# Kernel optimization log

Hardware: AMD Instinct MI355X
Metric: run time of the kernel (lower is better)

Reference implementation:

```python
import jax, jax.numpy as jnp
import numpy as np

N = 10000          # nodes
E = 200000         # edges (avg degree 20)
LAT = 128          # latent dim
NEXP = 8           # experts
NTYPE = 95         # atom types (hard-coded 95x0e in module)
M0, M1, M2 = 128, 64, 32          # node/out irreps muls for l=0,1,2 (dim 480)
E0, E1, E2 = 64, 32, 16           # edge irreps muls (dim 240)
C0, C1, C2 = M0 + E0, M1 + E1, M2 + E2   # concat channels per l
T0 = M0 + M1 + M2                 # gate-input scalars: 128 scalars + 96 gates
AVG_NEIGH = 20.0


def setup_inputs() -> dict:
    key = jax.random.key(0)
    ks = jax.random.split(key, 32)
    r = lambda i, sh: jax.random.normal(ks[i], sh, dtype=jnp.float32)
    return {
        "latents": r(0, (E, LAT)),
        "node_features": r(1, (N, M0 + 3 * M1 + 5 * M2)),
        "edge_features": r(2, (E, E0 + 3 * E1 + 5 * E2)),
        "edge_vector": r(3, (E, 3)),
        "mole_globals": r(4, (LAT,)),
        "wigner_D1": r(5, (E, 3, 3)),
        "wigner_D2": r(6, (E, 5, 5)),
        "node_onehot": jax.nn.one_hot(jax.random.randint(ks[7], (N,), 0, NTYPE), NTYPE, dtype=jnp.float32),
        "Wg": r(8, (LAT, NEXP)),
        "Wm": r(9, (LAT, NEXP)),
        "W0_e": r(10, (NEXP, C0, T0)), "W0_s": r(11, (C0, T0)),
        "W1_e": r(12, (NEXP, C1, M1)), "W1_s": r(13, (C1, M1)),
        "W2_e": r(14, (NEXP, C2, M2)), "W2_s": r(15, (C2, M2)),
        "Wp0": r(16, (M0, M0)), "bp0": jnp.zeros((M0,), jnp.float32),
        "Wp1": r(17, (M1, M1)), "Wp2": r(18, (M2, M2)),
        "Wenv": r(19, (LAT, M0 + M1 + M2)),
        "Woh0": r(20, (M0, NTYPE)), "Woh1": r(21, (M1, NTYPE)), "Woh2": r(22, (M2, NTYPE)),
        "atom_type": jax.random.randint(ks[23], (N,), 0, NTYPE),
        "edge_index": jax.random.randint(ks[24], (2, E), 0, N),
        "active_edges": jnp.arange(E),
    }


def _mix(x, We, Ws, g):
    """Latent(expert)-conditioned per-l channel mixing: y = x @ (sum_e g_e W_e + W_shared).
    Loops over the small fixed expert count; never materializes per-edge weight matrices."""
    xm = x if x.ndim == 3 else x[:, :, None]           # [a, c, m]
    y = jnp.einsum('acm,co->aom', xm, Ws)
    for e in range(NEXP):
        y = y + g[:, e, None, None] * jnp.einsum('acm,co->aom', xm, We[e])
    y = y * float(1.0 / np.sqrt(xm.shape[1]))
    return y[:, :, 0] if x.ndim == 2 else y


def reference(latents, node_features, edge_features, edge_vector, mole_globals,
              wigner_D1, wigner_D2, node_onehot, Wg, Wm,
              W0_e, W0_s, W1_e, W1_s, W2_e, W2_s,
              Wp0, bp0, Wp1, Wp2, Wenv, Woh0, Woh1, Woh2,
              atom_type, edge_index, active_edges):
    edge_center = edge_index[0][active_edges]
    lat = latents[active_edges]
    # gather node features along edges, split irreps blocks
    xn = node_features[edge_center]                         # [Ea, 480]
    n0 = xn[:, :M0]
    n1 = xn[:, M0:M0 + 3 * M1].reshape(-1, M1, 3)
    n2 = xn[:, M0 + 3 * M1:].reshape(-1, M2, 5)
    e0 = edge_features[:, :E0]
    e1 = edge_features[:, E0:E0 + 3 * E1].reshape(-1, E1, 3)
    e2 = edge_features[:, E0 + 3 * E1:].reshape(-1, E2, 5)
    x0 = jnp.concatenate([n0, e0], axis=1)                  # [Ea, C0]
    x1 = jnp.concatenate([n1, e1], axis=1)                  # [Ea, C1, 3]
    x2 = jnp.concatenate([n2, e2], axis=1)                  # [Ea, C2, 5]
    # latent + molecular-global conditioned expert gates
    gates = jax.nn.softmax(lat @ Wg + mole_globals @ Wm, axis=-1)   # [Ea, NEXP]
    # SO(2)-style TP: rotate l>0 blocks into edge frame (Wigner-D), mix channels, rotate back
    x1r = jnp.einsum('amn,acn->acm', wigner_D1, x1)
    x2r = jnp.einsum('amn,acn->acm', wigner_D2, x2)
    t0 = _mix(x0, W0_e, W0_s, gates)                        # [Ea, T0]
    t1 = jnp.einsum('anm,aom->aon', wigner_D1, _mix(x1r, W1_e, W1_s, gates))
    t2 = jnp.einsum('anm,aom->aon', wigner_D2, _mix(x2r, W2_e, W2_s, gates))
    # Gate nonlinearity: silu scalars, sigmoid gates scale l>0 channels
    s = jax.nn.silu(t0[:, :M0])
    v1 = t1 * jax.nn.sigmoid(t0[:, M0:M0 + M1])[:, :, None]
    v2 = t2 * jax.nn.sigmoid(t0[:, M0 + M1:])[:, :, None]
    # lin_post: per-l equivariant linear (bias only on scalars), fan-in normalized
    s = s @ Wp0 * float(1.0 / np.sqrt(M0)) + bp0
    v1 = jnp.einsum('acm,co->aom', v1, Wp1) * float(1.0 / np.sqrt(M1))
    v2 = jnp.einsum('acm,co->aom', v2, Wp2) * float(1.0 / np.sqrt(M2))
    # E3ElementLinear: per-channel weights generated from latents
    w = lat @ Wenv * float(1.0 / np.sqrt(LAT))              # [Ea, M0+M1+M2]
    s = s * w[:, :M0]
    v1 = v1 * w[:, M0:M0 + M1, None]
    v2 = v2 * w[:, M0 + M1:, None]
    # scatter-reduce messages to nodes, normalize by rsqrt(avg_num_neighbors)
    norm = float(1.0 / np.sqrt(AVG_NEIGH))
    o0 = jax.ops.segment_sum(s, edge_center, num_segments=N) * norm
    o1 = jax.ops.segment_sum(v1, edge_center, num_segments=N) * norm
    o2 = jax.ops.segment_sum(v2, edge_center, num_segments=N) * norm
    # residual blend (res_update_params=0 -> u=sigmoid(0)=0.5), identity residual
    u = 0.5
    c_old = float(1.0 / np.sqrt(u * u + 1.0))
    c_new = u * c_old
    h0 = c_old * node_features[:, :M0] + c_new * o0
    h1 = c_old * node_features[:, M0:M0 + 3 * M1].reshape(N, M1, 3) + c_new * o1
    h2 = c_old * node_features[:, M0 + 3 * M1:].reshape(N, M2, 5) + c_new * o2
    # layer-onehot 'uvu' weighted TP with 95x0e, fan-in normalized, added residually
    invs = float(1.0 / np.sqrt(NTYPE))
    h0 = h0 + h0 * (node_onehot @ Woh0.T) * invs
    h1 = h1 + h1 * (node_onehot @ Woh1.T)[:, :, None] * invs
    h2 = h2 + h2 * (node_onehot @ Woh2.T)[:, :, None] * invs
    return jnp.concatenate([h0, h1.reshape(N, 3 * M1), h2.reshape(N, 5 * M2)], axis=1)
```

## Files before the change

### kernel.cpp

```cpp
#include <hip/hip_runtime.h>
#include <math.h>

namespace {

typedef __attribute__((ext_vector_type(8))) short short8;
typedef __attribute__((ext_vector_type(4))) float f32x4;

constexpr int kN   = 10000;
constexpr int kE   = 200000;
constexpr int kNT  = 95;
constexpr int kNFD = 480;

__device__ __forceinline__ ushort bf(float f) {
  union { float f; uint u; } c; c.f = f;
  uint r = c.u + 0x7FFF + ((c.u >> 16) & 1);
  return (ushort)(r >> 16);
}
__device__ __forceinline__ float fb(ushort u) {
  union { uint u; float f; } c; c.u = ((uint)u) << 16;
  return c.f;
}
__device__ __forceinline__ uint pk2(float a, float b) {
  return (uint)bf(a) | ((uint)bf(b) << 16);
}
// ... 282 lines not shown
          float av = (o < 128) ? (val/(1.f + __expf(-val)))
                               : (1.f/(1.f + __expf(-val)));
          outbf[(size_t)gr*N + o] = bf(av);
        } else {
          int a = gr/DIV;
          if (bias != nullptr) val += bias[o];
          float w = fb(wenvbf[(size_t)a*224 + WCOL + o]);
          val *= w*0.22360679774997896f;
          outbf[(size_t)gr*N + o] = bf(val);
        }
      }
    }
  }
}

template<int L>
__global__ __launch_bounds__(512)
void pv_k(const ushort* __restrict__ y, const ushort* __restrict__ t0act,
          const float* __restrict__ Dm, const ushort* __restrict__ Bpk,
          int rowsReal, float norm, const ushort* __restrict__ wenvbf,
          ushort* __restrict__ peout) {
  constexpr int DIV = (L == 1) ? 3 : 5;
  constexpr int K1  = (L == 1) ? 64 : 32;
  constexpr int NK  = K1/32;
  constexpr int N   = K1;
  constexpr int NT  = N/16;
  constexpr int CTW = NT/2;
  constexpr int LDA = K1 + 8;
  constexpr int WCOL = (L == 1) ? 128 : 192;
  constexpr int DSTR = (L == 1) ? 9 : 25;

  extern __shared__ char smraw[];
  ushort* Asm = (ushort*)smraw;

  const int tid = threadIdx.x;
  const int row0 = blockIdx.x*128;

  constexpr int C8 = K1/8;
  for (int u = tid; u < 128*C8; u += 512) {
    int r = u / C8, c8 = u - r*C8;
    int c0 = c8*8;
    int gr = row0 + r;
    uint4 v = {0u,0u,0u,0u};
    if (gr < rowsReal) {
      int a = gr/DIV, n = gr - a*DIV;
      const float* dd = Dm + (size_t)a*DSTR + n*DIV;
      short8 gt = *(const short8*)(t0act + (size_t)a*224 + WCOL + c0);
      float ov[8];
      if constexpr (L == 1) {
        short8 m0 = *(const short8*)(y + ((size_t)a*3 + 0)*64 + c0);
        short8 m1 = *(const short8*)(y + ((size_t)a*3 + 1)*64 + c0);
        short8 m2 = *(const short8*)(y + ((size_t)a*3 + 2)*64 + c0);
        float d0 = dd[0], d1 = dd[1], d2 = dd[2];
        #pragma unroll
        for (int j = 0; j < 8; ++j) {
          float s = d0*fb((ushort)m0[j]) + d1*fb((ushort)m1[j]) + d2*fb((ushort)m2[j]);
          ov[j] = s*fb((ushort)gt[j]);
        }
      } else {
        short8 m0 = *(const short8*)(y + ((size_t)a*5 + 0)*32 + c0);
        short8 m1 = *(const short8*)(y + ((size_t)a*5 + 1)*32 + c0);
        short8 m2 = *(const short8*)(y + ((size_t)a*5 + 2)*32 + c0);
        short8 m3 = *(const short8*)(y + ((size_t)a*5 + 3)*32 + c0);
        short8 m4 = *(const short8*)(y + ((size_t)a*5 + 4)*32 + c0);
        float d0 = dd[0], d1 = dd[1], d2 = dd[2], d3 = dd[3], d4 = dd[4];
        #pragma unroll
        for (int j = 0; j < 8; ++j) {
          float s = d0*fb((ushort)m0[j]) + d1*fb((ushort)m1[j])
                  + d2*fb((ushort)m2[j]) + d3*fb((ushort)m3[j])
                  + d4*fb((ushort)m4[j]);
          ov[j] = s*fb((ushort)gt[j]);
        }
      }
      v.x = pk2(ov[0], ov[1]); v.y = pk2(ov[2], ov[3]);
      v.z = pk2(ov[4], ov[5]); v.w = pk2(ov[6], ov[7]);
    }
    *(uint4*)(&Asm[r*LDA + c0]) = v;
  }
  __syncthreads();

  const int lane = tid & 63, wid = tid >> 6;
  const int cg = wid & 1, rg = wid >> 1;
  const int rbase = rg*32;
  const int lrow = lane & 15, lkb = lane >> 4;

  short8 af[2][NK];
  #pragma unroll
  for (int rt = 0; rt < 2; ++rt)
    #pragma unroll
    for (int kc = 0; kc < NK; ++kc)
      af[rt][kc] = *(const short8*)(&Asm[(rbase + rt*16 + lrow)*LDA + kc*32 + lkb*8]);

  f32x4 acc[2][CTW];
  #pragma unroll
  for (int rt = 0; rt < 2; ++rt)
    #pragma unroll
    for (int ct = 0; ct < CTW; ++ct)
      acc[rt][ct] = f32x4{0.f,0.f,0.f,0.f};

  __syncthreads();

  union BU { uint4 u; short8 s; };
  uint4* Bsm4 = (uint4*)smraw;
  const uint4* Bg4 = (const uint4*)Bpk;

  for (int u = tid; u < NT*NK*64; u += 512)
    Bsm4[u] = Bg4[u];
  __syncthreads();

  #pragma unroll
  for (int ct = 0; ct < CTW; ++ct) {
    int nt = cg*CTW + ct;
    #pragma unroll
    for (int kc = 0; kc < NK; ++kc) {
      BU b; b.u = Bsm4[(nt*NK + kc)*64 + lane];
      acc[0][ct] = __builtin_amdgcn_mfma_f32_16x16x32_bf16(af[0][kc], b.s, acc[0][ct], 0, 0, 0);
      acc[1][ct] = __builtin_amdgcn_mfma_f32_16x16x32_bf16(af[1][kc], b.s, acc[1][ct], 0, 0, 0);
    }
  }

  #pragma unroll
  for (int rt = 0; rt < 2; ++rt) {
    #pragma unroll
    for (int ct = 0; ct < CTW; ++ct) {
      #pragma unroll
      for (int q = 0; q < 4; ++q) {
        int gr = row0 + rbase + rt*16 + lkb*4 + q;
        if (gr >= rowsReal) continue;
        int o = (cg*CTW + ct)*16 + lrow;
        int a = gr/DIV;
        float val = acc[rt][ct][q]*norm;
        float w = fb(wenvbf[(size_t)a*224 + WCOL + o]);
        val *= w*0.22360679774997896f;
        peout[(size_t)gr*N + o] = bf(val);
      }
    }
  }
}

constexpr int T0SMB = 55808;

template<int C>
__device__ __forceinline__ void t0_phase(int e, int tid, int lane, int cg,
                                         int rbase, int lkb,
                                         const short8 (&af)[2][6],
                                         f32x4 (&acc)[2][7],
                                         const float* coefsm,
                                         uint4* Bsm4, const uint4* Bg4,
                                         uint4& rg0, uint4& rg1, uint4& rg2) {
  fastbar();
  const bool hasNext = !(e == 8 && C == 3);
  if (hasNext) {
    int ne = e + (C == 3 ? 1 : 0);
    int nc = (C + 1) & 3;
    const uint4* s = Bg4 + (size_t)ne*6144 + (size_t)nc*1536;
    rg0 = s[tid]; rg1 = s[tid + 512]; rg2 = s[tid + 1024];
  }
  float cf[2][4];
  #pragma unroll
  for (int rt = 0; rt < 2; ++rt)
    #pragma unroll
    for (int q = 0; q < 4; ++q)
      cf[rt][q] = coefsm[(rbase + rt*16 + lkb*4 + q)*9 + e];
  union BU { uint4 u; short8 s; };
  const uint4* bb = Bsm4 + (C & 1)*1536;
  {
    f32x4 z0 = {0.f,0.f,0.f,0.f}, z1 = {0.f,0.f,0.f,0.f};
    #pragma unroll
    for (int kc = 0; kc < 6; ++kc) {
      BU b; b.u = bb[(cg*6 + kc)*64 + lane];
      z0 = __builtin_amdgcn_mfma_f32_16x16x32_bf16(af[0][kc], b.s, z0, 0, 0, 0);
      z1 = __builtin_amdgcn_mfma_f32_16x16x32_bf16(af[1][kc], b.s, z1, 0, 0, 0);
    }
    #pragma unroll
    for (int q = 0; q < 4; ++q) {
      acc[0][2*C][q] += cf[0][q]*z0[q];
      acc[1][2*C][q] += cf[1][q]*z1[q];
    }
  }
  if constexpr (2*C + 1 < 7) {
    f32x4 z0 = {0.f,0.f,0.f,0.f}, z1 = {0.f,0.f,0.f,0.f};
    #pragma unroll
    for (int kc = 0; kc < 6; ++kc) {
      BU b; b.u = bb[((2 + cg)*6 + kc)*64 + lane];
      z0 = __builtin_amdgcn_mfma_f32_16x16x32_bf16(af[0][kc], b.s, z0, 0, 0, 0);
      z1 = __builtin_amdgcn_mfma_f32_16x16x32_bf16(af[1][kc], b.s, z1, 0, 0, 0);
    }
    #pragma unroll
    for (int q = 0; q < 4; ++q) {
      acc[0][2*C + 1][q] += cf[0][q]*z0[q];
      acc[1][2*C + 1][q] += cf[1][q]*z1[q];
    }
  }
  fastbar();
  if (hasNext) {
    uint4* d = Bsm4 + ((C + 1) & 1)*1536;
    d[tid] = rg0; d[tid + 512] = rg1; d[tid + 1024] = rg2;
  }
}

__global__ __launch_bounds__(512, 2)
void t0c_k(const float* __restrict__ nodef, const float* __restrict__ edgef,
           const int* __restrict__ eidx, const int* __restrict__ act,
           const ushort* __restrict__ Bpk, const ushort* __restrict__ Bp0,
           const float* __restrict__ coefg, const float* __restrict__ bp0f,
           const ushort* __restrict__ wenvbf,
           ushort* __restrict__ t0act, ushort* __restrict__ pe0) {
  extern __shared__ char smraw[];
  __shared__ int cenl[128];
  ushort* Asm = (ushort*)smraw;
  float* coefsm = (float*)(smraw + 51200);
  uint4* Bsm4 = (uint4*)smraw;
  const uint4* Bg4 = (const uint4*)Bpk;

  const int tid = threadIdx.x;
  const int row0 = blockIdx.x*128;

  if (tid < 128) {
    int gr = row0 + tid;
    cenl[tid] = (gr < kE) ? eidx[act[gr]] : 0;
  }
  __syncthreads();

  for (int u = tid; u < 128*24; u += 512) {
    int r = u/24, g = u - r*24;
    int c0 = g*8;
    int gr = row0 + r;
    uint4 v = {0u,0u,0u,0u};
    if (gr < kE) {
      const float* s = (g < 16) ? (nodef + (size_t)cenl[r]*kNFD + c0)
                                : (edgef + (size_t)gr*240 + (c0 - 128));
      float4 f0 = *(const float4*)s;
      float4 f1 = *(const float4*)(s + 4);
      v.x = pk2(f0.x, f0.y); v.y = pk2(f0.z, f0.w);
      v.z = pk2(f1.x, f1.y); v.w = pk2(f1.z, f1.w);
    }
    *(uint4*)(&Asm[r*200 + c0]) = v;
  }
  for (int u = tid; u < 128*9; u += 512) {
    int r = u/9, e = u - r*9;
    coefsm[r*9 + e] = coefg[(size_t)(row0 + r)*9 + e];
  }
  __syncthreads();

  const int lane = tid & 63, wid = tid >> 6;
  const int cg = wid & 1, rg = wid >> 1;
  const int rbase = rg*32;
  const int lrow = lane & 15, lkb = lane >> 4;

  short8 af[2][6];
  #pragma unroll
  for (int rt = 0; rt < 2; ++rt)
    #pragma unroll
    for (int kc = 0; kc < 6; ++kc)
      af[rt][kc] = *(const short8*)(&Asm[(rbase + rt*16 + lrow)*200 + kc*32 + lkb*8]);

  f32x4 acc[2][7];
  #pragma unroll
  for (int rt = 0; rt < 2; ++rt)
    #pragma unroll
    for (int ct = 0; ct < 7; ++ct)
      acc[rt][ct] = f32x4{0.f,0.f,0.f,0.f};

  __syncthreads();

  uint4 rg0, rg1, rg2;
  { const uint4* s = Bg4; rg0 = s[tid]; rg1 = s[tid + 512]; rg2 = s[tid + 1024]; }
  { uint4* d = Bsm4;      d[tid] = rg0; d[tid + 512] = rg1; d[tid + 1024] = rg2; }

  for (int e = 0; e < 9; ++e) {
    t0_phase<0>(e, tid, lane, cg, rbase, lkb, af, acc, coefsm, Bsm4, Bg4, rg0, rg1, rg2);
    t0_phase<1>(e, tid, lane, cg, rbase, lkb, af, acc, coefsm, Bsm4, Bg4, rg0, rg1, rg2);
    t0_phase<2>(e, tid, lane, cg, rbase, lkb, af, acc, coefsm, Bsm4, Bg4, rg0, rg1, rg2);
    t0_phase<3>(e, tid, lane, cg, rbase, lkb, af, acc, coefsm, Bsm4, Bg4, rg0, rg1, rg2);
  }

  ushort* A2 = (ushort*)smraw;
  #pragma unroll
  for (int rt = 0; rt < 2; ++rt) {
    #pragma unroll
    for (int ct = 0; ct < 7; ++ct) {
      int o = (2*ct + cg)*16 + lrow;
      #pragma unroll
      for (int q = 0; q < 4; ++q) {
        int rloc = rbase + rt*16 + lkb*4 + q;
        int gr = row0 + rloc;
        float val = acc[rt][ct][q]*0.07216878364870323f;
        if (o < 128) {
          A2[rloc*136 + o] = bf(val/(1.f + __expf(-val)));
        } else if (gr < kE) {
          t0act[(size_t)gr*224 + o] = bf(1.f/(1.f + __expf(-val)));
        }
      }
    }
  }
  fastbar();

  short8 af2[2][4];
  #pragma unroll
  for (int rt = 0; rt < 2; ++rt)
    #pragma unroll
    for (int kc = 0; kc < 4; ++kc)
      af2[rt][kc] = *(const short8*)(&A2[(rbase + rt*16 + lrow)*136 + kc*32 + lkb*8]);

  union BU { uint4 u; short8 s; };
  const uint4* Bg0 = (const uint4*)Bp0;
  f32x4 acc2[2][4];
  #pragma unroll
  for (int rt = 0; rt < 2; ++rt)
    #pragma unroll
    for (int ct = 0; ct < 4; ++ct)
      acc2[rt][ct] = f32x4{0.f,0.f,0.f,0.f};

  #pragma unroll
  for (int ct = 0; ct < 4; ++ct) {
    int nt = cg*4 + ct;
    #pragma unroll
    for (int kc = 0; kc < 4; ++kc) {
      BU b; b.u = Bg0[(nt*4 + kc)*64 + lane];
      acc2[0][ct] = __builtin_amdgcn_mfma_f32_16x16x32_bf16(af2[0][kc], b.s, acc2[0][ct], 0, 0, 0);
      acc2[1][ct] = __builtin_amdgcn_mfma_f32_16x16x32_bf16(af2[1][kc], b.s, acc2[1][ct], 0, 0, 0);
    }
  }

  #pragma unroll
  for (int rt = 0; rt < 2; ++rt) {
    #pragma unroll
    for (int ct = 0; ct < 4; ++ct) {
      int o = (cg*4 + ct)*16 + lrow;
      float bia = bp0f[o];
      #pragma unroll
      for (int q = 0; q < 4; ++q) {
        int gr = row0 + rbase + rt*16 + lkb*4 + q;
        if (gr >= kE) continue;
        float v = acc2[rt][ct][q]*0.08838834764831845f + bia;
        v *= fb(wenvbf[(size_t)gr*224 + o])*0.22360679774997896f;
        pe0[(size_t)gr*128 + o] = bf(v);
      }
    }
  }
}

constexpr int ych_smbytes(int K1, int NK, int NT) {
  int a = 128*(K1 + 8)*2;
  int b = 2*NT*NK*1024;
  int u = a > b ? a : b;
  return u + 128*9*4;
}

template<int DIV, int K1, int NK, int NT, int FUSE>
__global__ __launch_bounds__(512, 2)
void ychunk_k(const float* __restrict__ nodef, const float* __restrict__ edgef,
              const float* __restrict__ Dm, const int* __restrict__ eidx,
              const int* __restrict__ act, const ushort* __restrict__ Bpk,
              const float* __restrict__ coefg, int rowsReal, float norm,
              ushort* __restrict__ outbf) {
  constexpr int CTW = NT/2;
  constexpr int N   = NT*16;
  constexpr int LDA = K1 + 8;
  constexpr int ABYTES = 128*LDA*2;
  constexpr int BBYTES = 2*NT*NK*1024;
  constexpr int UNI = (ABYTES > BBYTES) ? ABYTES : BBYTES;
  constexpr int NB4 = NT*NK*64;
  constexpr int DSTR = (FUSE == 1) ? 9 : 25;

  extern __shared__ char smraw[];
  ushort* Asm = (ushort*)smraw;
  float* coefsm = (float*)(smraw + UNI);
  uint4* Bsm4 = (uint4*)smraw;
  const uint4* Bg4 = (const uint4*)Bpk;

  const int tid = threadIdx.x;
  const int row0 = blockIdx.x*128;

  constexpr int C8 = K1/8;
  for (int u = tid; u < 128*C8; u += 512) {
    int r = u / C8, c8 = u - r*C8;
    int c0 = c8*8;
    int gr = row0 + r;
    uint4 v = {0u,0u,0u,0u};
    if (gr < rowsReal) {
      int a = gr/DIV, mm = gr - a*DIV;
      int cen = eidx[act[a]];
      const float* dd = Dm + (size_t)a*DSTR + mm*DIV;
      if constexpr (FUSE == 1) {
        const float* s = (c8 < 8) ? (nodef + (size_t)cen*kNFD + 128 + c0*3)
                                  : (edgef + (size_t)a*240 + 64 + (c0 - 64)*3);
        float ld[24];
        #pragma unroll
        for (int q = 0; q < 6; ++q)
          *(float4*)(ld + q*4) = *(const float4*)(s + q*4);
        float d0 = dd[0], d1 = dd[1], d2 = dd[2];
        float ov[8];
        #pragma unroll
        for (int j = 0; j < 8; ++j)
          ov[j] = d0*ld[3*j] + d1*ld[3*j + 1] + d2*ld[3*j + 2];
        v.x = pk2(ov[0], ov[1]); v.y = pk2(ov[2], ov[3]);
        v.z = pk2(ov[4], ov[5]); v.w = pk2(ov[6], ov[7]);
      } else {
        if (c0 < 48) {
// ... 77 lines not shown
      }
      #pragma unroll
      for (int q = 0; q < 4; ++q) {
        acc[0][ct][q] += cf[0][q]*z0[q];
        acc[1][ct][q] += cf[1][q]*z1[q];
      }
    }
    fastbar();
    if (e + 1 < 9) {
      uint4* d = Bsm4 + ((e + 1) & 1)*NB4;
      if (tid < NB4) d[tid] = pf0;
      if constexpr (NB4 > 512) { if (tid + 512 < NB4) d[tid + 512] = pf1; }
    }
  }

  #pragma unroll
  for (int rt = 0; rt < 2; ++rt) {
    #pragma unroll
    for (int ct = 0; ct < CTW; ++ct) {
      #pragma unroll
      for (int q = 0; q < 4; ++q) {
        int gr = row0 + rbase + rt*16 + lkb*4 + q;
        if (gr >= rowsReal) continue;
        int o = (cg*CTW + ct)*16 + lrow;
        outbf[(size_t)gr*N + o] = bf(acc[rt][ct][q]*norm);
      }
    }
  }
}

__global__ __launch_bounds__(256)
void gather_k(const float* __restrict__ nodef, const float* __restrict__ onehot,
              const float* __restrict__ Woh0, const float* __restrict__ Woh1,
              const float* __restrict__ Woh2,
              const int* __restrict__ rowptr, const int* __restrict__ elist,
              const ushort* __restrict__ pe0, const ushort* __restrict__ pe1,
              const ushort* __restrict__ pe2, float* __restrict__ out) {
  __shared__ int tn;
  const int n = blockIdx.x;
  const int t = threadIdx.x;
// ... 27 lines not shown
    if (j < 128)      f = Woh0[j*kNT + ty];
    else if (j < 320) f = Woh1[((j - 128)/3)*kNT + ty];
    else              f = Woh2[((j - 320)/5)*kNT + ty];
    out[idx] = h*(1.f + f*invs);
  }
}

constexpr size_t OFF_CNT  = 0;
constexpr size_t OFF_CUR  = 40000;
constexpr size_t OFF_RP   = 80000;
constexpr size_t OFF_EL   = 120064;
constexpr size_t OFF_PACK = 1000000;
constexpr size_t OFF_COEF = 19200000;
constexpr size_t OFF_MGL  = 26402304;
constexpr size_t OFF_PE0  = 168031232;
constexpr size_t OFF_X2R  = 219264000;
constexpr size_t OFF_WENV = 347272192;
constexpr size_t OFF_T0A  = 436900864;
constexpr size_t OFF_Y1   = 526529536;
constexpr size_t OFF_Y2   = 603354112;

}

extern "C" void kernel_launch(void* const* d_in, const int* in_sizes, int n_in,
                              void* d_out, int out_size, void* d_ws, size_t ws_size,
                              hipStream_t stream) {
  (void)in_sizes; (void)n_in; (void)out_size; (void)ws_size;
  const float* latents = (const float*)d_in[0];
  const float* nodef   = (const float*)d_in[1];
  const float* edgef   = (const float*)d_in[2];
  const float* mg      = (const float*)d_in[4];
  const float* D1      = (const float*)d_in[5];
  const float* D2      = (const float*)d_in[6];
  const float* onehot  = (const float*)d_in[7];
  const float* Wg      = (const float*)d_in[8];
// ... 13 lines not shown
  const float* Woh1    = (const float*)d_in[22];
  const float* Woh2    = (const float*)d_in[23];
  const int* eidx      = (const int*)d_in[25];
  const int* act       = (const int*)d_in[26];

  char* ws = (char*)d_ws;
  int*    cnt   = (int*)(ws + OFF_CNT);
  int*    cur   = (int*)(ws + OFF_CUR);
  int*    rp    = (int*)(ws + OFF_RP);
  int*    el    = (int*)(ws + OFF_EL);
  ushort* pk    = (ushort*)(ws + OFF_PACK);
  float*  coef  = (float*)(ws + OFF_COEF);
  float*  mgl   = (float*)(ws + OFF_MGL);
  ushort* wenv  = (ushort*)(ws + OFF_WENV);
  ushort* t0act = (ushort*)(ws + OFF_T0A);
  ushort* y1    = (ushort*)(ws + OFF_Y1);
  ushort* y2    = (ushort*)(ws + OFF_Y2);
  ushort* pe0   = (ushort*)(ws + OFF_PE0);
  ushort* pe1   = (ushort*)(ws + OFF_X2R);
  ushort* pe2   = (ushort*)(ws + OFF_Y1);
  float*  out   = (float*)d_out;

  hipMemsetAsync(cnt, 0, kN*sizeof(int), stream);
  hist_k<<<(kE + 255)/256, 256, 0, stream>>>(eidx, act, cnt);
  scan_k<<<1, 256, 0, stream>>>(cnt, rp, cur);
  scatter_k<<<(kE + 255)/256, 256, 0, stream>>>(eidx, act, cur, el);

  pack_k<<<(PKTOT + 255)/256, 256, 0, stream>>>(W0e, W0s, W1e, W1s, W2e, W2s,
                                                Wenv, Wp0, Wp1, Wp2, pk);
  mgl_k<<<1, 64, 0, stream>>>(mg, Wm, mgl);

  coef_k<<<kE/32, 256, 0, stream>>>(latents, mgl, Wg, act, coef);

  {
    auto kp = gemm_k<1,128,4,224,1,0,true>;
    int smb = gemm_smbytes(128,4,224,1);
    hipFuncSetAttribute((const void*)kp, hipFuncAttributeMaxDynamicSharedMemorySize, smb);
    kp<<<1563, 512, smb, stream>>>(
        nullptr, latents, act, 128, pk + PKENV, nullptr, kE, 0.08838834764831845f,
        wenv, nullptr, nullptr, 0);
  }
  {
    auto kp = ychunk_k<3,96,3,4,1>;
    int smb = ych_smbytes(96,3,4);
    hipFuncSetAttribute((const void*)kp, hipFuncAttributeMaxDynamicSharedMemorySize, smb);
    kp<<<4688, 512, smb, stream>>>(
        nodef, edgef, D1, eidx, act, pk + PK1, coef, 3*kE,
        0.10206207261596577f, y1);
  }
  {
    auto kp = ychunk_k<5,64,2,2,2>;
    int smb = ych_smbytes(64,2,2);
    hipFuncSetAttribute((const void*)kp, hipFuncAttributeMaxDynamicSharedMemorySize, smb);
    kp<<<7813, 512, smb, stream>>>(
        nodef, edgef, D2, eidx, act, pk + PK2, coef, 5*kE,
        0.14433756729740643f, y2);
  }

  {
    hipFuncSetAttribute((const void*)t0c_k,
                        hipFuncAttributeMaxDynamicSharedMemorySize, T0SMB);
    t0c_k<<<1563, 512, T0SMB, stream>>>(nodef, edgef, eidx, act,
                                        pk + PK0, pk + PKP0, coef,
                                        bp0, wenv, t0act, pe0);
  }

  {
    auto kp = pv_k<1>;
    int smb = gemm_smbytes(64,2,64,1);
    hipFuncSetAttribute((const void*)kp, hipFuncAttributeMaxDynamicSharedMemorySize, smb);
    kp<<<4688, 512, smb, stream>>>(
        y1, t0act, D1, pk + PKP1, 3*kE, 0.125f, wenv, pe1);
  }
  {
    auto kp = pv_k<2>;
    int smb = gemm_smbytes(32,1,32,1);
    hipFuncSetAttribute((const void*)kp, hipFuncAttributeMaxDynamicSharedMemorySize, smb);
    kp<<<7813, 512, smb, stream>>>(
        y2, t0act, D2, pk + PKP2, 5*kE, 0.17677669529663687f, wenv, pe2);
  }

  gather_k<<<kN, 256, 0, stream>>>(nodef, onehot, Woh0, Woh1, Woh2,
                                   rp, el, pe0, pe1, pe2, out);
}
```

Baseline: 1.272 ms.

## Fuse expert-mix chunk GEMM with rotate-back projection for l=1,2 paths

Merges the ychunk kernels (expert-weighted mixing of l=1/l=2 channels) with the pv kernels (Wigner back-rotation, gating, post-projection and envelope scaling) into one ypv kernel per l. The intermediate y tensors now stay in shared memory instead of round-tripping through global memory. To keep each edge's m-components inside one block, blocks cover 126 or 125 rows (multiples of 3 or 5) rather than 128, so a few MFMA rows are wasted. Occupancy is capped at one block per CU via launch bounds, and the larger shared footprint may reduce latency hiding.

```diff
diff --git a/kernel.cpp b/kernel.cpp
--- a/kernel.cpp
+++ b/kernel.cpp
@@ -320,27 +320,54 @@
   }
 }
 
+constexpr int ypv_smbytes(int K1, int NK, int NT) {
+  int a = 128*(K1 + 8)*2;
+  int b = 2*NT*NK*1024;
+  int y = 128*(NT*16 + 8)*2;
+  int u = a > b ? a : b;
+  u = u > y ? u : y;
+  return u + 128*9*4;
+}
+
 template<int L>
-__global__ __launch_bounds__(512)
-void pv_k(const ushort* __restrict__ y, const ushort* __restrict__ t0act,
-          const float* __restrict__ Dm, const ushort* __restrict__ Bpk,
-          int rowsReal, float norm, const ushort* __restrict__ wenvbf,
-          ushort* __restrict__ peout) {
-  constexpr int DIV = (L == 1) ? 3 : 5;
-  constexpr int K1  = (L == 1) ? 64 : 32;
-  constexpr int NK  = K1/32;
-  constexpr int N   = K1;
-  constexpr int NT  = N/16;
-  constexpr int CTW = NT/2;
-  constexpr int LDA = K1 + 8;
+__global__ __launch_bounds__(512, 1)
+void ypv_k(const float* __restrict__ nodef, const float* __restrict__ edgef,
+           const float* __restrict__ Dm, const int* __restrict__ eidx,
+           const int* __restrict__ act, const ushort* __restrict__ Bpk,
+           const ushort* __restrict__ Bp, const float* __restrict__ coefg,
+           const ushort* __restrict__ t0act, const ushort* __restrict__ wenvbf,
+           ushort* __restrict__ peout) {
+  constexpr int DIV  = (L == 1) ? 3 : 5;
+  constexpr int K1   = (L == 1) ? 96 : 64;
+  constexpr int NK   = K1/32;
+  constexpr int NT   = (L == 1) ? 4 : 2;
+  constexpr int N    = NT*16;
+  constexpr int CTW  = NT/2;
+  constexpr int LDA  = K1 + 8;
+  constexpr int RR   = (L == 1) ? 126 : 125;
+  constexpr int DSTR = (L == 1) ? 9 : 25;
   constexpr int WCOL = (L == 1) ? 128 : 192;
-  constexpr int DSTR = (L == 1) ? 9 : 25;
+  constexpr int NB4  = NT*NK*64;
+  constexpr int LDY  = N + 8;
+  constexpr int NK2  = N/32;
+  constexpr int ABYTES = 128*LDA*2;
+  constexpr int BBYTES = 2*NB4*16;
+  constexpr int UNI0 = (ABYTES > BBYTES) ? ABYTES : BBYTES;
+  constexpr int YBYTES = 128*LDY*2;
+  constexpr int UNI = (UNI0 > YBYTES) ? UNI0 : YBYTES;
+
+  const float norm1 = (L == 1) ? 0.10206207261596577f : 0.14433756729740643f;
+  const float norm2 = (L == 1) ? 0.125f : 0.17677669529663687f;
+  const int rowsTotal = (L == 1) ? 3*kE : 5*kE;
 
   extern __shared__ char smraw[];
   ushort* Asm = (ushort*)smraw;
+  float* coefsm = (float*)(smraw + UNI);
+  uint4* Bsm4 = (uint4*)smraw;
+  const uint4* Bg4 = (const uint4*)Bpk;
 
   const int tid = threadIdx.x;
-  const int row0 = blockIdx.x*128;
+  const int row0 = blockIdx.x*RR;
 
   constexpr int C8 = K1/8;
   for (int u = tid; u < 128*C8; u += 512) {
@@ -348,348 +375,11 @@
     int c0 = c8*8;
     int gr = row0 + r;
     uint4 v = {0u,0u,0u,0u};
-    if (gr < rowsReal) {
-      int a = gr/DIV, n = gr - a*DIV;
-      const float* dd = Dm + (size_t)a*DSTR + n*DIV;
-      short8 gt = *(const short8*)(t0act + (size_t)a*224 + WCOL + c0);
-      float ov[8];
-      if constexpr (L == 1) {
-        short8 m0 = *(const short8*)(y + ((size_t)a*3 + 0)*64 + c0);
-        short8 m1 = *(const short8*)(y + ((size_t)a*3 + 1)*64 + c0);
-        short8 m2 = *(const short8*)(y + ((size_t)a*3 + 2)*64 + c0);
-        float d0 = dd[0], d1 = dd[1], d2 = dd[2];
-        #pragma unroll
-        for (int j = 0; j < 8; ++j) {
-          float s = d0*fb((ushort)m0[j]) + d1*fb((ushort)m1[j]) + d2*fb((ushort)m2[j]);
-          ov[j] = s*fb((ushort)gt[j]);
-        }
-      } else {
-        short8 m0 = *(const short8*)(y + ((size_t)a*5 + 0)*32 + c0);
-        short8 m1 = *(const short8*)(y + ((size_t)a*5 + 1)*32 + c0);
-        short8 m2 = *(const short8*)(y + ((size_t)a*5 + 2)*32 + c0);
-        short8 m3 = *(const short8*)(y + ((size_t)a*5 + 3)*32 + c0);
-        short8 m4 = *(const short8*)(y + ((size_t)a*5 + 4)*32 + c0);
-        float d0 = dd[0], d1 = dd[1], d2 = dd[2], d3 = dd[3], d4 = dd[4];
-        #pragma unroll
-        for (int j = 0; j < 8; ++j) {
-          float s = d0*fb((ushort)m0[j]) + d1*fb((ushort)m1[j])
-                  + d2*fb((ushort)m2[j]) + d3*fb((ushort)m3[j])
-                  + d4*fb((ushort)m4[j]);
-          ov[j] = s*fb((ushort)gt[j]);
-        }
-      }
-      v.x = pk2(ov[0], ov[1]); v.y = pk2(ov[2], ov[3]);
-      v.z = pk2(ov[4], ov[5]); v.w = pk2(ov[6], ov[7]);
-    }
-    *(uint4*)(&Asm[r*LDA + c0]) = v;
-  }
-  __syncthreads();
-
-  const int lane = tid & 63, wid = tid >> 6;
-  const int cg = wid & 1, rg = wid >> 1;
-  const int rbase = rg*32;
-  const int lrow = lane & 15, lkb = lane >> 4;
-
-  short8 af[2][NK];
-  #pragma unroll
-  for (int rt = 0; rt < 2; ++rt)
-    #pragma unroll
-    for (int kc = 0; kc < NK; ++kc)
-      af[rt][kc] = *(const short8*)(&Asm[(rbase + rt*16 + lrow)*LDA + kc*32 + lkb*8]);
-
-  f32x4 acc[2][CTW];
-  #pragma unroll
-  for (int rt = 0; rt < 2; ++rt)
-    #pragma unroll
-    for (int ct = 0; ct < CTW; ++ct)
-      acc[rt][ct] = f32x4{0.f,0.f,0.f,0.f};
-
-  __syncthreads();
-
-  union BU { uint4 u; short8 s; };
-  uint4* Bsm4 = (uint4*)smraw;
-  const uint4* Bg4 = (const uint4*)Bpk;
-
-  for (int u = tid; u < NT*NK*64; u += 512)
-    Bsm4[u] = Bg4[u];
-  __syncthreads();
-
-  #pragma unroll
-  for (int ct = 0; ct < CTW; ++ct) {
-    int nt = cg*CTW + ct;
-    #pragma unroll
-    for (int kc = 0; kc < NK; ++kc) {
-      BU b; b.u = Bsm4[(nt*NK + kc)*64 + lane];
-      acc[0][ct] = __builtin_amdgcn_mfma_f32_16x16x32_bf16(af[0][kc], b.s, acc[0][ct], 0, 0, 0);
-      acc[1][ct] = __builtin_amdgcn_mfma_f32_16x16x32_bf16(af[1][kc], b.s, acc[1][ct], 0, 0, 0);
-    }
-  }
-
-  #pragma unroll
-  for (int rt = 0; rt < 2; ++rt) {
-    #pragma unroll
-    for (int ct = 0; ct < CTW; ++ct) {
-      #pragma unroll
-      for (int q = 0; q < 4; ++q) {
-        int gr = row0 + rbase + rt*16 + lkb*4 + q;
-        if (gr >= rowsReal) continue;
-        int o = (cg*CTW + ct)*16 + lrow;
-        int a = gr/DIV;
-        float val = acc[rt][ct][q]*norm;
-        float w = fb(wenvbf[(size_t)a*224 + WCOL + o]);
-        val *= w*0.22360679774997896f;
-        peout[(size_t)gr*N + o] = bf(val);
-      }
-    }
-  }
-}
-
-constexpr int T0SMB = 55808;
-
-template<int C>
-__device__ __forceinline__ void t0_phase(int e, int tid, int lane, int cg,
-                                         int rbase, int lkb,
-                                         const short8 (&af)[2][6],
-                                         f32x4 (&acc)[2][7],
-                                         const float* coefsm,
-                                         uint4* Bsm4, const uint4* Bg4,
-                                         uint4& rg0, uint4& rg1, uint4& rg2) {
-  fastbar();
-  const bool hasNext = !(e == 8 && C == 3);
-  if (hasNext) {
-    int ne = e + (C == 3 ? 1 : 0);
-    int nc = (C + 1) & 3;
-    const uint4* s = Bg4 + (size_t)ne*6144 + (size_t)nc*1536;
-    rg0 = s[tid]; rg1 = s[tid + 512]; rg2 = s[tid + 1024];
-  }
-  float cf[2][4];
-  #pragma unroll
-  for (int rt = 0; rt < 2; ++rt)
-    #pragma unroll
-    for (int q = 0; q < 4; ++q)
-      cf[rt][q] = coefsm[(rbase + rt*16 + lkb*4 + q)*9 + e];
-  union BU { uint4 u; short8 s; };
-  const uint4* bb = Bsm4 + (C & 1)*1536;
-  {
-    f32x4 z0 = {0.f,0.f,0.f,0.f}, z1 = {0.f,0.f,0.f,0.f};
-    #pragma unroll
-    for (int kc = 0; kc < 6; ++kc) {
-      BU b; b.u = bb[(cg*6 + kc)*64 + lane];
-      z0 = __builtin_amdgcn_mfma_f32_16x16x32_bf16(af[0][kc], b.s, z0, 0, 0, 0);
-      z1 = __builtin_amdgcn_mfma_f32_16x16x32_bf16(af[1][kc], b.s, z1, 0, 0, 0);
-    }
-    #pragma unroll
-    for (int q = 0; q < 4; ++q) {
-      acc[0][2*C][q] += cf[0][q]*z0[q];
-      acc[1][2*C][q] += cf[1][q]*z1[q];
-    }
-  }
-  if constexpr (2*C + 1 < 7) {
-    f32x4 z0 = {0.f,0.f,0.f,0.f}, z1 = {0.f,0.f,0.f,0.f};
-    #pragma unroll
-    for (int kc = 0; kc < 6; ++kc) {
-      BU b; b.u = bb[((2 + cg)*6 + kc)*64 + lane];
-      z0 = __builtin_amdgcn_mfma_f32_16x16x32_bf16(af[0][kc], b.s, z0, 0, 0, 0);
-      z1 = __builtin_amdgcn_mfma_f32_16x16x32_bf16(af[1][kc], b.s, z1, 0, 0, 0);
-    }
-    #pragma unroll
-    for (int q = 0; q < 4; ++q) {
-      acc[0][2*C + 1][q] += cf[0][q]*z0[q];
-      acc[1][2*C + 1][q] += cf[1][q]*z1[q];
-    }
-  }
-  fastbar();
-  if (hasNext) {
-    uint4* d = Bsm4 + ((C + 1) & 1)*1536;
-    d[tid] = rg0; d[tid + 512] = rg1; d[tid + 1024] = rg2;
-  }
-}
-
-__global__ __launch_bounds__(512, 2)
-void t0c_k(const float* __restrict__ nodef, const float* __restrict__ edgef,
-           const int* __restrict__ eidx, const int* __restrict__ act,
-           const ushort* __restrict__ Bpk, const ushort* __restrict__ Bp0,
-           const float* __restrict__ coefg, const float* __restrict__ bp0f,
-           const ushort* __restrict__ wenvbf,
-           ushort* __restrict__ t0act, ushort* __restrict__ pe0) {
-  extern __shared__ char smraw[];
-  __shared__ int cenl[128];
-  ushort* Asm = (ushort*)smraw;
-  float* coefsm = (float*)(smraw + 51200);
-  uint4* Bsm4 = (uint4*)smraw;
-  const uint4* Bg4 = (const uint4*)Bpk;
-
-  const int tid = threadIdx.x;
-  const int row0 = blockIdx.x*128;
-
-  if (tid < 128) {
-    int gr = row0 + tid;
-    cenl[tid] = (gr < kE) ? eidx[act[gr]] : 0;
-  }
-  __syncthreads();
-
-  for (int u = tid; u < 128*24; u += 512) {
-    int r = u/24, g = u - r*24;
-    int c0 = g*8;
-    int gr = row0 + r;
-    uint4 v = {0u,0u,0u,0u};
-    if (gr < kE) {
-      const float* s = (g < 16) ? (nodef + (size_t)cenl[r]*kNFD + c0)
-                                : (edgef + (size_t)gr*240 + (c0 - 128));
-      float4 f0 = *(const float4*)s;
-      float4 f1 = *(const float4*)(s + 4);
-      v.x = pk2(f0.x, f0.y); v.y = pk2(f0.z, f0.w);
-      v.z = pk2(f1.x, f1.y); v.w = pk2(f1.z, f1.w);
-    }
-    *(uint4*)(&Asm[r*200 + c0]) = v;
-  }
-  for (int u = tid; u < 128*9; u += 512) {
-    int r = u/9, e = u - r*9;
-    coefsm[r*9 + e] = coefg[(size_t)(row0 + r)*9 + e];
-  }
-  __syncthreads();
-
-  const int lane = tid & 63, wid = tid >> 6;
-  const int cg = wid & 1, rg = wid >> 1;
-  const int rbase = rg*32;
-  const int lrow = lane & 15, lkb = lane >> 4;
-
-  short8 af[2][6];
-  #pragma unroll
-  for (int rt = 0; rt < 2; ++rt)
-    #pragma unroll
-    for (int kc = 0; kc < 6; ++kc)
-      af[rt][kc] = *(const short8*)(&Asm[(rbase + rt*16 + lrow)*200 + kc*32 + lkb*8]);
-
-  f32x4 acc[2][7];
-  #pragma unroll
-  for (int rt = 0; rt < 2; ++rt)
-    #pragma unroll
-    for (int ct = 0; ct < 7; ++ct)
-      acc[rt][ct] = f32x4{0.f,0.f,0.f,0.f};
-
-  __syncthreads();
-
-  uint4 rg0, rg1, rg2;
-  { const uint4* s = Bg4; rg0 = s[tid]; rg1 = s[tid + 512]; rg2 = s[tid + 1024]; }
-  { uint4* d = Bsm4;      d[tid] = rg0; d[tid + 512] = rg1; d[tid + 1024] = rg2; }
-
-  for (int e = 0; e < 9; ++e) {
-    t0_phase<0>(e, tid, lane, cg, rbase, lkb, af, acc, coefsm, Bsm4, Bg4, rg0, rg1, rg2);
-    t0_phase<1>(e, tid, lane, cg, rbase, lkb, af, acc, coefsm, Bsm4, Bg4, rg0, rg1, rg2);
-    t0_phase<2>(e, tid, lane, cg, rbase, lkb, af, acc, coefsm, Bsm4, Bg4, rg0, rg1, rg2);
-    t0_phase<3>(e, tid, lane, cg, rbase, lkb, af, acc, coefsm, Bsm4, Bg4, rg0, rg1, rg2);
-  }
-
-  ushort* A2 = (ushort*)smraw;
-  #pragma unroll
-  for (int rt = 0; rt < 2; ++rt) {
-    #pragma unroll
-    for (int ct = 0; ct < 7; ++ct) {
-      int o = (2*ct + cg)*16 + lrow;
-      #pragma unroll
-      for (int q = 0; q < 4; ++q) {
-        int rloc = rbase + rt*16 + lkb*4 + q;
-        int gr = row0 + rloc;
-        float val = acc[rt][ct][q]*0.07216878364870323f;
-        if (o < 128) {
-          A2[rloc*136 + o] = bf(val/(1.f + __expf(-val)));
-        } else if (gr < kE) {
-          t0act[(size_t)gr*224 + o] = bf(1.f/(1.f + __expf(-val)));
-        }
-      }
-    }
-  }
-  fastbar();
-
-  short8 af2[2][4];
-  #pragma unroll
-  for (int rt = 0; rt < 2; ++rt)
-    #pragma unroll
-    for (int kc = 0; kc < 4; ++kc)
-      af2[rt][kc] = *(const short8*)(&A2[(rbase + rt*16 + lrow)*136 + kc*32 + lkb*8]);
-
-  union BU { uint4 u; short8 s; };
-  const uint4* Bg0 = (const uint4*)Bp0;
-  f32x4 acc2[2][4];
-  #pragma unroll
-  for (int rt = 0; rt < 2; ++rt)
-    #pragma unroll
-    for (int ct = 0; ct < 4; ++ct)
-      acc2[rt][ct] = f32x4{0.f,0.f,0.f,0.f};
-
-  #pragma unroll
-  for (int ct = 0; ct < 4; ++ct) {
-    int nt = cg*4 + ct;
-    #pragma unroll
-    for (int kc = 0; kc < 4; ++kc) {
-      BU b; b.u = Bg0[(nt*4 + kc)*64 + lane];
-      acc2[0][ct] = __builtin_amdgcn_mfma_f32_16x16x32_bf16(af2[0][kc], b.s, acc2[0][ct], 0, 0, 0);
-      acc2[1][ct] = __builtin_amdgcn_mfma_f32_16x16x32_bf16(af2[1][kc], b.s, acc2[1][ct], 0, 0, 0);
-    }
-  }
-
-  #pragma unroll
-  for (int rt = 0; rt < 2; ++rt) {
-    #pragma unroll
-    for (int ct = 0; ct < 4; ++ct) {
-      int o = (cg*4 + ct)*16 + lrow;
-      float bia = bp0f[o];
-      #pragma unroll
-      for (int q = 0; q < 4; ++q) {
-        int gr = row0 + rbase + rt*16 + lkb*4 + q;
-        if (gr >= kE) continue;
-        float v = acc2[rt][ct][q]*0.08838834764831845f + bia;
-        v *= fb(wenvbf[(size_t)gr*224 + o])*0.22360679774997896f;
-        pe0[(size_t)gr*128 + o] = bf(v);
-      }
-    }
-  }
-}
-
-constexpr int ych_smbytes(int K1, int NK, int NT) {
-  int a = 128*(K1 + 8)*2;
-  int b = 2*NT*NK*1024;
-  int u = a > b ? a : b;
-  return u + 128*9*4;
-}
-
-template<int DIV, int K1, int NK, int NT, int FUSE>
-__global__ __launch_bounds__(512, 2)
-void ychunk_k(const float* __restrict__ nodef, const float* __restrict__ edgef,
-              const float* __restrict__ Dm, const int* __restrict__ eidx,
-              const int* __restrict__ act, const ushort* __restrict__ Bpk,
-              const float* __restrict__ coefg, int rowsReal, float norm,
-              ushort* __restrict__ outbf) {
-  constexpr int CTW = NT/2;
-  constexpr int N   = NT*16;
-  constexpr int LDA = K1 + 8;
-  constexpr int ABYTES = 128*LDA*2;
-  constexpr int BBYTES = 2*NT*NK*1024;
-  constexpr int UNI = (ABYTES > BBYTES) ? ABYTES : BBYTES;
-  constexpr int NB4 = NT*NK*64;
-  constexpr int DSTR = (FUSE == 1) ? 9 : 25;
-
-  extern __shared__ char smraw[];
-  ushort* Asm = (ushort*)smraw;
-  float* coefsm = (float*)(smraw + UNI);
-  uint4* Bsm4 = (uint4*)smraw;
-  const uint4* Bg4 = (const uint4*)Bpk;
-
-  const int tid = threadIdx.x;
-  const int row0 = blockIdx.x*128;
-
-  constexpr int C8 = K1/8;
-  for (int u = tid; u < 128*C8; u += 512) {
-    int r = u / C8, c8 = u - r*C8;
-    int c0 = c8*8;
-    int gr = row0 + r;
-    uint4 v = {0u,0u,0u,0u};
-    if (gr < rowsReal) {
+    if (gr < rowsTotal) {
       int a = gr/DIV, mm = gr - a*DIV;
       int cen = eidx[act[a]];
       const float* dd = Dm + (size_t)a*DSTR + mm*DIV;
-      if constexpr (FUSE == 1) {
+      if constexpr (L == 1) {
         const float* s = (c8 < 8) ? (nodef + (size_t)cen*kNFD + 128 + c0*3)
                                   : (edgef + (size_t)a*240 + 64 + (c0 - 64)*3);
         float ld[24];
@@ -797,16 +487,300 @@
     }
   }
 
+  ushort* yl = (ushort*)smraw;
   #pragma unroll
   for (int rt = 0; rt < 2; ++rt) {
     #pragma unroll
     for (int ct = 0; ct < CTW; ++ct) {
+      int o = (cg*CTW + ct)*16 + lrow;
+      #pragma unroll
+      for (int q = 0; q < 4; ++q) {
+        int r = rbase + rt*16 + lkb*4 + q;
+        yl[r*LDY + o] = bf(acc[rt][ct][q]*norm1);
+      }
+    }
+  }
+  fastbar();
+
+  short8 af2[2][NK2];
+  #pragma unroll
+  for (int rt = 0; rt < 2; ++rt) {
+    int r2 = rbase + rt*16 + lrow;
+    int gr = row0 + r2;
+    bool valid = (r2 < RR) && (gr < rowsTotal);
+    float dd[DIV];
+    int rb = 0;
+    const ushort* gtp = nullptr;
+    if (valid) {
+      int a = gr/DIV, n = gr - a*DIV;
+      rb = r2 - n;
+      #pragma unroll
+      for (int m = 0; m < DIV; ++m) dd[m] = Dm[(size_t)a*DSTR + n*DIV + m];
+      gtp = t0act + (size_t)a*224 + WCOL;
+    }
+    #pragma unroll
+    for (int kc = 0; kc < NK2; ++kc) {
+      int c0 = kc*32 + lkb*8;
+      short8 frag = {0,0,0,0,0,0,0,0};
+      if (valid) {
+        short8 gt = *(const short8*)(gtp + c0);
+        float ov[8];
+        #pragma unroll
+        for (int j = 0; j < 8; ++j) ov[j] = 0.f;
+        #pragma unroll
+        for (int m = 0; m < DIV; ++m) {
+          short8 ym = *(const short8*)(&yl[(rb + m)*LDY + c0]);
+          #pragma unroll
+          for (int j = 0; j < 8; ++j) ov[j] += dd[m]*fb((ushort)ym[j]);
+        }
+        uint4 pkd;
+        pkd.x = pk2(ov[0]*fb((ushort)gt[0]), ov[1]*fb((ushort)gt[1]));
+        pkd.y = pk2(ov[2]*fb((ushort)gt[2]), ov[3]*fb((ushort)gt[3]));
+        pkd.z = pk2(ov[4]*fb((ushort)gt[4]), ov[5]*fb((ushort)gt[5]));
+        pkd.w = pk2(ov[6]*fb((ushort)gt[6]), ov[7]*fb((ushort)gt[7]));
+        union { uint4 u; short8 s; } cv; cv.u = pkd;
+        frag = cv.s;
+      }
+      af2[rt][kc] = frag;
+    }
+  }
+
+  const uint4* Bgp = (const uint4*)Bp;
+  f32x4 acc2[2][CTW];
+  #pragma unroll
+  for (int rt = 0; rt < 2; ++rt)
+    #pragma unroll
+    for (int ct = 0; ct < CTW; ++ct)
+      acc2[rt][ct] = f32x4{0.f,0.f,0.f,0.f};
+
+  #pragma unroll
+  for (int ct = 0; ct < CTW; ++ct) {
+    int nt = cg*CTW + ct;
+    #pragma unroll
+    for (int kc = 0; kc < NK2; ++kc) {
+      BU b; b.u = Bgp[(nt*NK2 + kc)*64 + lane];
+      acc2[0][ct] = __builtin_amdgcn_mfma_f32_16x16x32_bf16(af2[0][kc], b.s, acc2[0][ct], 0, 0, 0);
+      acc2[1][ct] = __builtin_amdgcn_mfma_f32_16x16x32_bf16(af2[1][kc], b.s, acc2[1][ct], 0, 0, 0);
+    }
+  }
+
+  #pragma unroll
+  for (int rt = 0; rt < 2; ++rt) {
+    #pragma unroll
+    for (int ct = 0; ct < CTW; ++ct) {
+      int o = (cg*CTW + ct)*16 + lrow;
+      #pragma unroll
+      for (int q = 0; q < 4; ++q) {
+        int r2 = rbase + rt*16 + lkb*4 + q;
+        int gr = row0 + r2;
+        if (r2 >= RR || gr >= rowsTotal) continue;
+        int a = gr/DIV;
+        float val = acc2[rt][ct][q]*norm2;
+        val *= fb(wenvbf[(size_t)a*224 + WCOL + o])*0.22360679774997896f;
+        peout[(size_t)gr*N + o] = bf(val);
+      }
+    }
+  }
+}
+
+constexpr int T0SMB = 55808;
+
+template<int C>
+__device__ __forceinline__ void t0_phase(int e, int tid, int lane, int cg,
+                                         int rbase, int lkb,
+                                         const short8 (&af)[2][6],
+                                         f32x4 (&acc)[2][7],
+                                         const float* coefsm,
+                                         uint4* Bsm4, const uint4* Bg4,
+                                         uint4& rg0, uint4& rg1, uint4& rg2) {
+  fastbar();
+  const bool hasNext = !(e == 8 && C == 3);
+  if (hasNext) {
+    int ne = e + (C == 3 ? 1 : 0);
+    int nc = (C + 1) & 3;
+    const uint4* s = Bg4 + (size_t)ne*6144 + (size_t)nc*1536;
+    rg0 = s[tid]; rg1 = s[tid + 512]; rg2 = s[tid + 1024];
+  }
+  float cf[2][4];
+  #pragma unroll
+  for (int rt = 0; rt < 2; ++rt)
+    #pragma unroll
+    for (int q = 0; q < 4; ++q)
+      cf[rt][q] = coefsm[(rbase + rt*16 + lkb*4 + q)*9 + e];
+  union BU { uint4 u; short8 s; };
+  const uint4* bb = Bsm4 + (C & 1)*1536;
+  {
+    f32x4 z0 = {0.f,0.f,0.f,0.f}, z1 = {0.f,0.f,0.f,0.f};
+    #pragma unroll
+    for (int kc = 0; kc < 6; ++kc) {
+      BU b; b.u = bb[(cg*6 + kc)*64 + lane];
+      z0 = __builtin_amdgcn_mfma_f32_16x16x32_bf16(af[0][kc], b.s, z0, 0, 0, 0);
+      z1 = __builtin_amdgcn_mfma_f32_16x16x32_bf16(af[1][kc], b.s, z1, 0, 0, 0);
+    }
+    #pragma unroll
+    for (int q = 0; q < 4; ++q) {
+      acc[0][2*C][q] += cf[0][q]*z0[q];
+      acc[1][2*C][q] += cf[1][q]*z1[q];
+    }
+  }
+  if constexpr (2*C + 1 < 7) {
+    f32x4 z0 = {0.f,0.f,0.f,0.f}, z1 = {0.f,0.f,0.f,0.f};
+    #pragma unroll
+    for (int kc = 0; kc < 6; ++kc) {
+      BU b; b.u = bb[((2 + cg)*6 + kc)*64 + lane];
+      z0 = __builtin_amdgcn_mfma_f32_16x16x32_bf16(af[0][kc], b.s, z0, 0, 0, 0);
+      z1 = __builtin_amdgcn_mfma_f32_16x16x32_bf16(af[1][kc], b.s, z1, 0, 0, 0);
+    }
+    #pragma unroll
+    for (int q = 0; q < 4; ++q) {
+      acc[0][2*C + 1][q] += cf[0][q]*z0[q];
+      acc[1][2*C + 1][q] += cf[1][q]*z1[q];
+    }
+  }
+  fastbar();
+  if (hasNext) {
+    uint4* d = Bsm4 + ((C + 1) & 1)*1536;
+    d[tid] = rg0; d[tid + 512] = rg1; d[tid + 1024] = rg2;
+  }
+}
+
+__global__ __launch_bounds__(512, 2)
+void t0c_k(const float* __restrict__ nodef, const float* __restrict__ edgef,
+           const int* __restrict__ eidx, const int* __restrict__ act,
+           const ushort* __restrict__ Bpk, const ushort* __restrict__ Bp0,
+           const float* __restrict__ coefg, const float* __restrict__ bp0f,
+           const ushort* __restrict__ wenvbf,
+           ushort* __restrict__ t0act, ushort* __restrict__ pe0) {
+  extern __shared__ char smraw[];
+  __shared__ int cenl[128];
+  ushort* Asm = (ushort*)smraw;
+  float* coefsm = (float*)(smraw + 51200);
+  uint4* Bsm4 = (uint4*)smraw;
+  const uint4* Bg4 = (const uint4*)Bpk;
+
+  const int tid = threadIdx.x;
+  const int row0 = blockIdx.x*128;
+
+  if (tid < 128) {
+    int gr = row0 + tid;
+    cenl[tid] = (gr < kE) ? eidx[act[gr]] : 0;
+  }
+  __syncthreads();
+
+  for (int u = tid; u < 128*24; u += 512) {
+    int r = u/24, g = u - r*24;
+    int c0 = g*8;
+    int gr = row0 + r;
+    uint4 v = {0u,0u,0u,0u};
+    if (gr < kE) {
+      const float* s = (g < 16) ? (nodef + (size_t)cenl[r]*kNFD + c0)
+                                : (edgef + (size_t)gr*240 + (c0 - 128));
+      float4 f0 = *(const float4*)s;
+      float4 f1 = *(const float4*)(s + 4);
+      v.x = pk2(f0.x, f0.y); v.y = pk2(f0.z, f0.w);
+      v.z = pk2(f1.x, f1.y); v.w = pk2(f1.z, f1.w);
+    }
+    *(uint4*)(&Asm[r*200 + c0]) = v;
+  }
+  for (int u = tid; u < 128*9; u += 512) {
+    int r = u/9, e = u - r*9;
+    coefsm[r*9 + e] = coefg[(size_t)(row0 + r)*9 + e];
+  }
+  __syncthreads();
+
+  const int lane = tid & 63, wid = tid >> 6;
+  const int cg = wid & 1, rg = wid >> 1;
+  const int rbase = rg*32;
+  const int lrow = lane & 15, lkb = lane >> 4;
+
+  short8 af[2][6];
+  #pragma unroll
+  for (int rt = 0; rt < 2; ++rt)
+    #pragma unroll
+    for (int kc = 0; kc < 6; ++kc)
+      af[rt][kc] = *(const short8*)(&Asm[(rbase + rt*16 + lrow)*200 + kc*32 + lkb*8]);
+
+  f32x4 acc[2][7];
+  #pragma unroll
+  for (int rt = 0; rt < 2; ++rt)
+    #pragma unroll
+    for (int ct = 0; ct < 7; ++ct)
+      acc[rt][ct] = f32x4{0.f,0.f,0.f,0.f};
+
+  __syncthreads();
+
+  uint4 rg0, rg1, rg2;
+  { const uint4* s = Bg4; rg0 = s[tid]; rg1 = s[tid + 512]; rg2 = s[tid + 1024]; }
+  { uint4* d = Bsm4;      d[tid] = rg0; d[tid + 512] = rg1; d[tid + 1024] = rg2; }
+
+  for (int e = 0; e < 9; ++e) {
+    t0_phase<0>(e, tid, lane, cg, rbase, lkb, af, acc, coefsm, Bsm4, Bg4, rg0, rg1, rg2);
+    t0_phase<1>(e, tid, lane, cg, rbase, lkb, af, acc, coefsm, Bsm4, Bg4, rg0, rg1, rg2);
+    t0_phase<2>(e, tid, lane, cg, rbase, lkb, af, acc, coefsm, Bsm4, Bg4, rg0, rg1, rg2);
+    t0_phase<3>(e, tid, lane, cg, rbase, lkb, af, acc, coefsm, Bsm4, Bg4, rg0, rg1, rg2);
+  }
+
+  ushort* A2 = (ushort*)smraw;
+  #pragma unroll
+  for (int rt = 0; rt < 2; ++rt) {
+    #pragma unroll
+    for (int ct = 0; ct < 7; ++ct) {
+      int o = (2*ct + cg)*16 + lrow;
+      #pragma unroll
+      for (int q = 0; q < 4; ++q) {
+        int rloc = rbase + rt*16 + lkb*4 + q;
+        int gr = row0 + rloc;
+        float val = acc[rt][ct][q]*0.07216878364870323f;
+        if (o < 128) {
+          A2[rloc*136 + o] = bf(val/(1.f + __expf(-val)));
+        } else if (gr < kE) {
+          t0act[(size_t)gr*224 + o] = bf(1.f/(1.f + __expf(-val)));
+        }
+      }
+    }
+  }
+  fastbar();
+
+  short8 af2[2][4];
+  #pragma unroll
+  for (int rt = 0; rt < 2; ++rt)
+    #pragma unroll
+    for (int kc = 0; kc < 4; ++kc)
+      af2[rt][kc] = *(const short8*)(&A2[(rbase + rt*16 + lrow)*136 + kc*32 + lkb*8]);
+
+  union BU { uint4 u; short8 s; };
+  const uint4* Bg0 = (const uint4*)Bp0;
+  f32x4 acc2[2][4];
+  #pragma unroll
+  for (int rt = 0; rt < 2; ++rt)
+    #pragma unroll
+    for (int ct = 0; ct < 4; ++ct)
+      acc2[rt][ct] = f32x4{0.f,0.f,0.f,0.f};
+
+  #pragma unroll
+  for (int ct = 0; ct < 4; ++ct) {
+    int nt = cg*4 + ct;
+    #pragma unroll
+    for (int kc = 0; kc < 4; ++kc) {
+      BU b; b.u = Bg0[(nt*4 + kc)*64 + lane];
+      acc2[0][ct] = __builtin_amdgcn_mfma_f32_16x16x32_bf16(af2[0][kc], b.s, acc2[0][ct], 0, 0, 0);
+      acc2[1][ct] = __builtin_amdgcn_mfma_f32_16x16x32_bf16(af2[1][kc], b.s, acc2[1][ct], 0, 0, 0);
+    }
+  }
+
+  #pragma unroll
+  for (int rt = 0; rt < 2; ++rt) {
+    #pragma unroll
+    for (int ct = 0; ct < 4; ++ct) {
+      int o = (cg*4 + ct)*16 + lrow;
+      float bia = bp0f[o];
       #pragma unroll
       for (int q = 0; q < 4; ++q) {
         int gr = row0 + rbase + rt*16 + lkb*4 + q;
-        if (gr >= rowsReal) continue;
-        int o = (cg*CTW + ct)*16 + lrow;
-        outbf[(size_t)gr*N + o] = bf(acc[rt][ct][q]*norm);
+        if (gr >= kE) continue;
+        float v = acc2[rt][ct][q]*0.08838834764831845f + bia;
+        v *= fb(wenvbf[(size_t)gr*224 + o])*0.22360679774997896f;
+        pe0[(size_t)gr*128 + o] = bf(v);
       }
     }
   }
@@ -864,11 +838,10 @@
 constexpr size_t OFF_COEF = 19200000;
 constexpr size_t OFF_MGL  = 26402304;
 constexpr size_t OFF_PE0  = 168031232;
-constexpr size_t OFF_X2R  = 219264000;
+constexpr size_t OFF_PE1  = 219264000;
 constexpr size_t OFF_WENV = 347272192;
 constexpr size_t OFF_T0A  = 436900864;
-constexpr size_t OFF_Y1   = 526529536;
-constexpr size_t OFF_Y2   = 603354112;
+constexpr size_t OFF_PE2  = 526529536;
 
 }
 
@@ -912,11 +885,9 @@
   float*  mgl   = (float*)(ws + OFF_MGL);
   ushort* wenv  = (ushort*)(ws + OFF_WENV);
   ushort* t0act = (ushort*)(ws + OFF_T0A);
-  ushort* y1    = (ushort*)(ws + OFF_Y1);
-  ushort* y2    = (ushort*)(ws + OFF_Y2);
   ushort* pe0   = (ushort*)(ws + OFF_PE0);
-  ushort* pe1   = (ushort*)(ws + OFF_X2R);
-  ushort* pe2   = (ushort*)(ws + OFF_Y1);
+  ushort* pe1   = (ushort*)(ws + OFF_PE1);
+  ushort* pe2   = (ushort*)(ws + OFF_PE2);
   float*  out   = (float*)d_out;
 
   hipMemsetAsync(cnt, 0, kN*sizeof(int), stream);
@@ -927,7 +898,6 @@
   pack_k<<<(PKTOT + 255)/256, 256, 0, stream>>>(W0e, W0s, W1e, W1s, W2e, W2s,
                                                 Wenv, Wp0, Wp1, Wp2, pk);
   mgl_k<<<1, 64, 0, stream>>>(mg, Wm, mgl);
-
   coef_k<<<kE/32, 256, 0, stream>>>(latents, mgl, Wg, act, coef);
 
   {
@@ -938,22 +908,6 @@
         nullptr, latents, act, 128, pk + PKENV, nullptr, kE, 0.08838834764831845f,
         wenv, nullptr, nullptr, 0);
   }
-  {
-    auto kp = ychunk_k<3,96,3,4,1>;
-    int smb = ych_smbytes(96,3,4);
-    hipFuncSetAttribute((const void*)kp, hipFuncAttributeMaxDynamicSharedMemorySize, smb);
-    kp<<<4688, 512, smb, stream>>>(
-        nodef, edgef, D1, eidx, act, pk + PK1, coef, 3*kE,
-        0.10206207261596577f, y1);
-  }
-  {
-    auto kp = ychunk_k<5,64,2,2,2>;
-    int smb = ych_smbytes(64,2,2);
-    hipFuncSetAttribute((const void*)kp, hipFuncAttributeMaxDynamicSharedMemorySize, smb);
-    kp<<<7813, 512, smb, stream>>>(
-        nodef, edgef, D2, eidx, act, pk + PK2, coef, 5*kE,
-        0.14433756729740643f, y2);
-  }
 
   {
     hipFuncSetAttribute((const void*)t0c_k,
@@ -964,18 +918,20 @@
   }
 
   {
-    auto kp = pv_k<1>;
-    int smb = gemm_smbytes(64,2,64,1);
+    auto kp = ypv_k<1>;
+    int smb = ypv_smbytes(96, 3, 4);
     hipFuncSetAttribute((const void*)kp, hipFuncAttributeMaxDynamicSharedMemorySize, smb);
-    kp<<<4688, 512, smb, stream>>>(
-        y1, t0act, D1, pk + PKP1, 3*kE, 0.125f, wenv, pe1);
+    int grid = (3*kE + 125)/126;
+    kp<<<grid, 512, smb, stream>>>(nodef, edgef, D1, eidx, act,
+                                   pk + PK1, pk + PKP1, coef, t0act, wenv, pe1);
   }
   {
-    auto kp = pv_k<2>;
-    int smb = gemm_smbytes(32,1,32,1);
+    auto kp = ypv_k<2>;
+    int smb = ypv_smbytes(64, 2, 2);
     hipFuncSetAttribute((const void*)kp, hipFuncAttributeMaxDynamicSharedMemorySize, smb);
-    kp<<<7813, 512, smb, stream>>>(
-        y2, t0act, D2, pk + PKP2, 5*kE, 0.17677669529663687f, wenv, pe2);
+    int grid = (5*kE + 124)/125;
+    kp<<<grid, 512, smb, stream>>>(nodef, edgef, D2, eidx, act,
+                                   pk + PK2, pk + PKP2, coef, t0act, wenv, pe2);
   }
 
   gather_k<<<kN, 256, 0, stream>>>(nodef, onehot, Woh0, Woh1, Woh2,
```

Measured after the change: 1.401 ms. +10.1%, slower.
